# Kernel optimization log

Hardware: AMD Instinct MI355X
Metric: run time of the kernel (lower is better)

Reference implementation:

```python
import jax, jax.numpy as jnp
import numpy as np

HIDDEN = 32
INPUT = 1
B, T = 512, 2048


def setup_inputs() -> dict:
    key = jax.random.key(0)
    ks = jax.random.split(key, 12)
    s = 1.0 / np.sqrt(HIDDEN)  # torch RNN init scale
    u = lambda k, shape: jax.random.uniform(k, shape, jnp.float32, -s, s)
    return {
        "x": jax.random.normal(ks[0], (B, T, INPUT), jnp.float32),
        "hidden": jax.random.normal(ks[1], (2, B, HIDDEN), jnp.float32),
        # layer 0 (input_size=1)
        "W_ih0": u(ks[2], (HIDDEN, INPUT)),
        "W_hh0": u(ks[3], (HIDDEN, HIDDEN)),
        "b_ih0": u(ks[4], (HIDDEN,)),
        "b_hh0": u(ks[5], (HIDDEN,)),
        # layer 1 (input_size=HIDDEN)
        "W_ih1": u(ks[6], (HIDDEN, HIDDEN)),
        "W_hh1": u(ks[7], (HIDDEN, HIDDEN)),
        "b_ih1": u(ks[8], (HIDDEN,)),
        "b_hh1": u(ks[9], (HIDDEN,)),
        # output projection fc: Linear(HIDDEN, 1)
        "W_fc": u(ks[10], (1, HIDDEN)),
        "b_fc": u(ks[11], (1,)),
    }


def reference(x, hidden, W_ih0, W_hh0, b_ih0, b_hh0, W_ih1, W_hh1, b_ih1, b_hh1, W_fc, b_fc):
    # x: [B, T, 1], hidden: [2, B, H]. Vanilla tanh RNN, 2 layers, batch_first.
    xs = jnp.swapaxes(x, 0, 1)  # [T, B, 1] for scan over time

    def step(carry, x_t):
        h0, h1 = carry
        h0 = jnp.tanh(x_t @ W_ih0.T + b_ih0 + h0 @ W_hh0.T + b_hh0)
        h1 = jnp.tanh(h0 @ W_ih1.T + b_ih1 + h1 @ W_hh1.T + b_hh1)
        return (h0, h1), h1

    (h0_f, h1_f), ys = jax.lax.scan(step, (hidden[0], hidden[1]), xs)  # ys: [T, B, H]
    # fc applied per timestep in torch loop == one batched matmul here (same math)
    outs = ys @ W_fc.T + b_fc                     # [T, B, 1]
    outs = jnp.swapaxes(outs, 0, 1)               # [B, T, 1]
    hidden_out = jnp.stack([h0_f, h1_f], axis=0)  # [2, B, H] (detached in torch)
    return outs, hidden_out
```

## Files before the change

kernel.cpp:

```cpp
#include <hip/hip_runtime.h>

#define TT 2048
#define HH 32
#define BB 512
#define SCL 2.8853900817779268f

typedef float f32x2 __attribute__((ext_vector_type(2)));

#define PKFMA(acc, a, b) asm("v_pk_fma_f32 %0, %1, %2, %0" : "+v"(acc) : "v"(a), "v"(b))

__device__ __forceinline__ float tanh2(float s) {
    float e;
    asm("v_exp_f32 %0, %1" : "=v"(e) : "v"(s));
    float r = __builtin_amdgcn_rcpf(e + 1.0f);
    return fmaf(-2.0f, r, 1.0f);
}

__global__ __launch_bounds__(64) void rnn_fused(
    const float* __restrict__ x,
    const float* __restrict__ hid,
    const float* __restrict__ W_ih0,
    const float* __restrict__ W_hh0,
    const float* __restrict__ b_ih0,
    const float* __restrict__ b_hh0,
    const float* __restrict__ W_ih1,
    const float* __restrict__ W_hh1,
    const float* __restrict__ b_ih1,
    const float* __restrict__ b_hh1,
    const float* __restrict__ W_fc,
    const float* __restrict__ b_fc,
    float* __restrict__ out)
{
    const int lane   = (int)threadIdx.x;
    const int i      = lane & 31;
    const bool lower = lane < 32;
    const int b      = (int)blockIdx.x;

    __shared__ __align__(16) float sh[64];
    __shared__ float xs[32];

    const float* rowA = lower ? (W_hh0 + i * HH) : (W_ih1 + i * HH);
    const float* rowB = lower ? W_fc             : (W_hh1 + i * HH);
    const float  sclB = lower ? 1.0f : SCL;
    f32x2 wA[16], wB[16];
#pragma unroll
    for (int j = 0; j < 16; ++j) {
        wA[j] = f32x2{SCL * rowA[2 * j], SCL * rowA[2 * j + 1]};
        wB[j] = f32x2{sclB * rowB[2 * j], sclB * rowB[2 * j + 1]};
    }
    const float wx   = lower ? (SCL * W_ih0[i]) : 0.0f;
    const float bias = SCL * (lower ? (b_ih0[i] + b_hh0[i])
                                    : (b_ih1[i] + b_hh1[i]));
    const float sel  = lower ? 0.0f : 1.0f;
    const float bfc  = b_fc[0];

    const float h_init = lower ? hid[b * HH + i] : hid[BB * HH + b * HH + i];
    sh[lane] = h_init;

    const float* xrow = x + b * TT;
    float* orow = out + b * TT;

    xs[i] = xrow[i];
    float xnxt = xrow[32 + i];

    float hn = h_init;

    float4 q[16];
    auto LOADQ = [&]() {
#pragma unroll
        for (int m = 0; m < 16; ++m) q[m] = *(const float4*)&sh[4 * m];
    };
    LOADQ();

    auto STEP = [&](int kidx, bool do_store, int off) {
        float xv = xs[kidx];
        f32x2 A0 = {bias, 0.f}, A1 = {0.f, 0.f};
        f32x2 B0 = {0.f, 0.f},  B1 = {0.f, 0.f};
#pragma unroll
        for (int m = 0; m < 8; ++m) {
            f32x2 qa = {q[m].x, q[m].y}, qb = {q[m].z, q[m].w};
            PKFMA(A0, wA[2 * m], qa);
            PKFMA(A1, wA[2 * m + 1], qb);
        }
#pragma unroll
        for (int m = 0; m < 8; ++m) {
            f32x2 qa = {q[8 + m].x, q[8 + m].y}, qb = {q[8 + m].z, q[8 + m].w};
            PKFMA(B0, wB[2 * m], qa);
            PKFMA(B1, wB[2 * m + 1], qb);
        }
        f32x2 As = A0 + A1, Bs = B0 + B1;
        float s1 = As.x + As.y;
        float s2 = Bs.x + Bs.y;
        float pre = fmaf(sel, s2, fmaf(wx, xv, s1));
        float h = tanh2(pre);
        sh[lane] = h;
        hn = h;
        if (do_store && lane == 0) orow[off] = s2 + bfc;
        LOADQ();
    };

    {
        float xv = xs[0];
        f32x2 A0 = {bias, 0.f}, A1 = {0.f, 0.f};
#pragma unroll
        for (int m = 0; m < 8; ++m) {
            f32x2 qa = {q[m].x, q[m].y}, qb = {q[m].z, q[m].w};
            PKFMA(A0, wA[2 * m], qa);
            PKFMA(A1, wA[2 * m + 1], qb);
        }
        f32x2 As = A0 + A1;
        float h0new = tanh2(fmaf(wx, xv, As.x + As.y));
        float hw = lower ? h0new : h_init;
        sh[lane] = hw;
        if (lower) hn = h0new;
        LOADQ();
    }

#pragma unroll
    for (int k = 1; k < 32; ++k) {
        STEP(k, k >= 2, k - 2);
    }
    xs[i] = xnxt;
    xnxt = xrow[64 + i];

    for (int tb = 1; tb < 64; ++tb) {
        const int base = tb * 32;
#pragma unroll
        for (int k = 0; k < 32; ++k) {
            STEP(k, true, base + k - 2);
        }
        xs[i] = xnxt;
        int nidx = (tb + 2) * 32 + i;
        if (nidx >= TT) nidx = TT - 1;
        xnxt = xrow[nidx];
    }

    const float h0_fin = hn;

    STEP(0, true, TT - 2);

    {
        f32x2 B0 = {0.f, 0.f}, B1 = {0.f, 0.f};
#pragma unroll
        for (int m = 0; m < 8; ++m) {
            f32x2 qa = {q[8 + m].x, q[8 + m].y}, qb = {q[8 + m].z, q[8 + m].w};
            PKFMA(B0, wB[2 * m], qa);
            PKFMA(B1, wB[2 * m + 1], qb);
        }
        f32x2 Bs = B0 + B1;
        if (lane == 0) orow[TT - 1] = (Bs.x + Bs.y) + bfc;
    }

    if (lower) {
        out[BB * TT + b * HH + i] = h0_fin;
    } else {
        out[BB * TT + BB * HH + b * HH + i] = hn;
    }
}

extern "C" void kernel_launch(void* const* d_in, const int* in_sizes, int n_in,
                              void* d_out, int out_size, void* d_ws, size_t ws_size,
                              hipStream_t stream) {
    const float* xp    = (const float*)d_in[0];
    const float* hid   = (const float*)d_in[1];
    const float* Wih0  = (const float*)d_in[2];
    const float* Whh0  = (const float*)d_in[3];
    const float* bih0  = (const float*)d_in[4];
    const float* bhh0  = (const float*)d_in[5];
    const float* Wih1  = (const float*)d_in[6];
    const float* Whh1  = (const float*)d_in[7];
    const float* bih1  = (const float*)d_in[8];
    const float* bhh1  = (const float*)d_in[9];
    const float* Wfc   = (const float*)d_in[10];
    const float* bfc   = (const float*)d_in[11];
    float* outp        = (float*)d_out;

    rnn_fused<<<BB, 64, 0, stream>>>(xp, hid, Wih0, Whh0, bih0, bhh0,
                                     Wih1, Whh1, bih1, bhh1, Wfc, bfc, outp);
}
```

Before: 372.9 us.

## Split each RNN step into two half-phases with separate LDS exchanges

Each timestep now runs as two phases. First, all 64 lanes compute the layer-0-style dot product and tanh, write the result to LDS and reload the lower half. Then they compute the second dot product, apply a second tanh, write to LDS and reload the upper half. Layer-0 lanes republish h0 so the skewed pipeline's data dependencies become shorter chains with interleaved LDS traffic. The cost is an extra tanh and extra LDS write/read round trips per step, and the wavefront-level ordering of LDS accesses without barriers is subtle.

Measured after the change: 446.8 us. +19.8%, slower.

```diff
diff --git a/kernel.cpp b/kernel.cpp
--- a/kernel.cpp
+++ b/kernel.cpp
@@ -51,7 +51,6 @@
     const float wx   = lower ? (SCL * W_ih0[i]) : 0.0f;
     const float bias = SCL * (lower ? (b_ih0[i] + b_hh0[i])
                                     : (b_ih1[i] + b_hh1[i]));
-    const float sel  = lower ? 0.0f : 1.0f;
     const float bfc  = b_fc[0];
 
     const float h_init = lower ? hid[b * HH + i] : hid[BB * HH + b * HH + i];
@@ -65,38 +64,45 @@
 
     float hn = h_init;
 
-    float4 q[16];
-    auto LOADQ = [&]() {
+    float4 a[8], bq[8];
 #pragma unroll
-        for (int m = 0; m < 16; ++m) q[m] = *(const float4*)&sh[4 * m];
-    };
-    LOADQ();
+    for (int m = 0; m < 8; ++m) a[m]  = *(const float4*)&sh[4 * m];
+#pragma unroll
+    for (int m = 0; m < 8; ++m) bq[m] = *(const float4*)&sh[32 + 4 * m];
 
-    auto STEP = [&](int kidx, bool do_store, int off) {
-        float xv = xs[kidx];
+    auto ITER = [&](int k, bool do_store, int off) {
+        float xv = xs[k];
         f32x2 A0 = {bias, 0.f}, A1 = {0.f, 0.f};
-        f32x2 B0 = {0.f, 0.f},  B1 = {0.f, 0.f};
 #pragma unroll
         for (int m = 0; m < 8; ++m) {
-            f32x2 qa = {q[m].x, q[m].y}, qb = {q[m].z, q[m].w};
+            f32x2 qa = {a[m].x, a[m].y}, qb = {a[m].z, a[m].w};
             PKFMA(A0, wA[2 * m], qa);
             PKFMA(A1, wA[2 * m + 1], qb);
         }
+        f32x2 As = A0 + A1;
+        float s1 = As.x + As.y;
+        float h0c = tanh2(fmaf(wx, xv, s1));
+        float ew = lower ? h0c : hn;
+        sh[lane] = ew;
+#pragma unroll
+        for (int m = 0; m < 8; ++m) a[m] = *(const float4*)&sh[4 * m];
+
+        f32x2 B0 = {0.f, 0.f}, B1 = {0.f, 0.f};
 #pragma unroll
         for (int m = 0; m < 8; ++m) {
-            f32x2 qa = {q[8 + m].x, q[8 + m].y}, qb = {q[8 + m].z, q[8 + m].w};
+            f32x2 qa = {bq[m].x, bq[m].y}, qb = {bq[m].z, bq[m].w};
             PKFMA(B0, wB[2 * m], qa);
             PKFMA(B1, wB[2 * m + 1], qb);
         }
-        f32x2 As = A0 + A1, Bs = B0 + B1;
-        float s1 = As.x + As.y;
+        f32x2 Bs = B0 + B1;
         float s2 = Bs.x + Bs.y;
-        float pre = fmaf(sel, s2, fmaf(wx, xv, s1));
-        float h = tanh2(pre);
-        sh[lane] = h;
-        hn = h;
+        float h1c = tanh2(s1 + s2);
+        float lw = lower ? h0c : h1c;
+        sh[lane] = lw;
+#pragma unroll
+        for (int m = 0; m < 8; ++m) bq[m] = *(const float4*)&sh[32 + 4 * m];
+        hn = lw;
         if (do_store && lane == 0) orow[off] = s2 + bfc;
-        LOADQ();
     };
 
     {
@@ -104,21 +110,22 @@
         f32x2 A0 = {bias, 0.f}, A1 = {0.f, 0.f};
 #pragma unroll
         for (int m = 0; m < 8; ++m) {
-            f32x2 qa = {q[m].x, q[m].y}, qb = {q[m].z, q[m].w};
+            f32x2 qa = {a[m].x, a[m].y}, qb = {a[m].z, a[m].w};
             PKFMA(A0, wA[2 * m], qa);
             PKFMA(A1, wA[2 * m + 1], qb);
         }
         f32x2 As = A0 + A1;
-        float h0new = tanh2(fmaf(wx, xv, As.x + As.y));
-        float hw = lower ? h0new : h_init;
-        sh[lane] = hw;
-        if (lower) hn = h0new;
-        LOADQ();
+        float h0c = tanh2(fmaf(wx, xv, As.x + As.y));
+        float ew = lower ? h0c : hn;
+        sh[lane] = ew;
+#pragma unroll
+        for (int m = 0; m < 8; ++m) a[m] = *(const float4*)&sh[4 * m];
+        hn = ew;
     }
 
 #pragma unroll
     for (int k = 1; k < 32; ++k) {
-        STEP(k, k >= 2, k - 2);
+        ITER(k, k >= 2, k - 2);
     }
     xs[i] = xnxt;
     xnxt = xrow[64 + i];
@@ -127,7 +134,7 @@
         const int base = tb * 32;
 #pragma unroll
         for (int k = 0; k < 32; ++k) {
-            STEP(k, true, base + k - 2);
+            ITER(k, true, base + k - 2);
         }
         xs[i] = xnxt;
         int nidx = (tb + 2) * 32 + i;
@@ -137,13 +144,13 @@
 
     const float h0_fin = hn;
 
-    STEP(0, true, TT - 2);
+    ITER(0, true, TT - 2);
 
     {
         f32x2 B0 = {0.f, 0.f}, B1 = {0.f, 0.f};
 #pragma unroll
         for (int m = 0; m < 8; ++m) {
-            f32x2 qa = {q[8 + m].x, q[8 + m].y}, qb = {q[8 + m].z, q[8 + m].w};
+            f32x2 qa = {bq[m].x, bq[m].y}, qb = {bq[m].z, bq[m].w};
             PKFMA(B0, wB[2 * m], qa);
             PKFMA(B1, wB[2 * m + 1], qb);
         }
```

## Process two batch rows per wavefront with interleaved independent recurrences

Applied to the files above, without the earlier changes.

Each 64-lane block now handles two batch elements, interleaving their time-step recurrences so that one chain's FMA/tanh/LDS latency can overlap with the other's. The grid is halved to 256 blocks, so each block reuses the same weight registers across two sequences. This raises ILP within the serial dependency chain but doubles register use for the q arrays. With 256 CUs on MI355X, halving the grid leaves fewer waves than CUs, so per-wave throughput must improve enough to make up for it.

After: 703.9 us. 88.8% more time.

```diff
diff --git a/kernel.cpp b/kernel.cpp
--- a/kernel.cpp
+++ b/kernel.cpp
@@ -34,10 +34,11 @@
     const int lane   = (int)threadIdx.x;
     const int i      = lane & 31;
     const bool lower = lane < 32;
-    const int b      = (int)blockIdx.x;
-
-    __shared__ __align__(16) float sh[64];
-    __shared__ float xs[32];
+    const int bA     = (int)blockIdx.x * 2;
+    const int bB     = bA + 1;
+
+    __shared__ __align__(16) float shA[64], shB[64];
+    __shared__ float xsA[32], xsB[32];
 
     const float* rowA = lower ? (W_hh0 + i * HH) : (W_ih1 + i * HH);
     const float* rowB = lower ? W_fc             : (W_hh1 + i * HH);
@@ -54,26 +55,32 @@
     const float sel  = lower ? 0.0f : 1.0f;
     const float bfc  = b_fc[0];
 
-    const float h_init = lower ? hid[b * HH + i] : hid[BB * HH + b * HH + i];
-    sh[lane] = h_init;
-
-    const float* xrow = x + b * TT;
-    float* orow = out + b * TT;
-
-    xs[i] = xrow[i];
-    float xnxt = xrow[32 + i];
-
-    float hn = h_init;
-
-    float4 q[16];
-    auto LOADQ = [&]() {
-#pragma unroll
-        for (int m = 0; m < 16; ++m) q[m] = *(const float4*)&sh[4 * m];
-    };
-    LOADQ();
-
-    auto STEP = [&](int kidx, bool do_store, int off) {
-        float xv = xs[kidx];
+    const float h_initA = lower ? hid[bA * HH + i] : hid[BB * HH + bA * HH + i];
+    const float h_initB = lower ? hid[bB * HH + i] : hid[BB * HH + bB * HH + i];
+    shA[lane] = h_initA;
+    shB[lane] = h_initB;
+
+    const float* xrowA = x + bA * TT;
+    const float* xrowB = x + bB * TT;
+    float* orowA = out + bA * TT;
+    float* orowB = out + bB * TT;
+
+    xsA[i] = xrowA[i];
+    xsB[i] = xrowB[i];
+    float xnxtA = xrowA[32 + i];
+    float xnxtB = xrowB[32 + i];
+
+    float hnA = h_initA, hnB = h_initB;
+
+    float4 qA[16], qB[16];
+#pragma unroll
+    for (int m = 0; m < 16; ++m) qA[m] = *(const float4*)&shA[4 * m];
+#pragma unroll
+    for (int m = 0; m < 16; ++m) qB[m] = *(const float4*)&shB[4 * m];
+
+    auto STEP = [&](float4* q, float& hn, float* shp, const float* xsp,
+                    float* orowp, int k, bool do_store, int off) {
+        float xv = xsp[k];
         f32x2 A0 = {bias, 0.f}, A1 = {0.f, 0.f};
         f32x2 B0 = {0.f, 0.f},  B1 = {0.f, 0.f};
 #pragma unroll
@@ -93,14 +100,16 @@
         float s2 = Bs.x + Bs.y;
         float pre = fmaf(sel, s2, fmaf(wx, xv, s1));
         float h = tanh2(pre);
-        sh[lane] = h;
+        shp[lane] = h;
         hn = h;
-        if (do_store && lane == 0) orow[off] = s2 + bfc;
-        LOADQ();
+        if (do_store && lane == 0) orowp[off] = s2 + bfc;
+#pragma unroll
+        for (int m = 0; m < 16; ++m) q[m] = *(const float4*)&shp[4 * m];
     };
 
-    {
-        float xv = xs[0];
+    auto PEEL = [&](float4* q, float& hn, float* shp, const float* xsp,
+                    float h_init_) {
+        float xv = xsp[0];
         f32x2 A0 = {bias, 0.f}, A1 = {0.f, 0.f};
 #pragma unroll
         for (int m = 0; m < 8; ++m) {
@@ -109,37 +118,44 @@
             PKFMA(A1, wA[2 * m + 1], qb);
         }
         f32x2 As = A0 + A1;
-        float h0new = tanh2(fmaf(wx, xv, As.x + As.y));
-        float hw = lower ? h0new : h_init;
-        sh[lane] = hw;
-        if (lower) hn = h0new;
-        LOADQ();
-    }
+        float h0c = tanh2(fmaf(wx, xv, As.x + As.y));
+        float ew = lower ? h0c : h_init_;
+        shp[lane] = ew;
+        hn = ew;
+#pragma unroll
+        for (int m = 0; m < 16; ++m) q[m] = *(const float4*)&shp[4 * m];
+    };
+    PEEL(qA, hnA, shA, xsA, h_initA);
+    PEEL(qB, hnB, shB, xsB, h_initB);
 
 #pragma unroll
     for (int k = 1; k < 32; ++k) {
-        STEP(k, k >= 2, k - 2);
-    }
-    xs[i] = xnxt;
-    xnxt = xrow[64 + i];
+        STEP(qA, hnA, shA, xsA, orowA, k, k >= 2, k - 2);
+        STEP(qB, hnB, shB, xsB, orowB, k, k >= 2, k - 2);
+    }
+    xsA[i] = xnxtA;  xnxtA = xrowA[64 + i];
+    xsB[i] = xnxtB;  xnxtB = xrowB[64 + i];
 
     for (int tb = 1; tb < 64; ++tb) {
         const int base = tb * 32;
 #pragma unroll
         for (int k = 0; k < 32; ++k) {
-            STEP(k, true, base + k - 2);
-        }
-        xs[i] = xnxt;
+            STEP(qA, hnA, shA, xsA, orowA, k, true, base + k - 2);
+            STEP(qB, hnB, shB, xsB, orowB, k, true, base + k - 2);
+        }
         int nidx = (tb + 2) * 32 + i;
         if (nidx >= TT) nidx = TT - 1;
-        xnxt = xrow[nidx];
-    }
-
-    const float h0_fin = hn;
-
-    STEP(0, true, TT - 2);
-
-    {
+        xsA[i] = xnxtA;  xnxtA = xrowA[nidx];
+        xsB[i] = xnxtB;  xnxtB = xrowB[nidx];
+    }
+
+    const float h0_finA = hnA;
+    const float h0_finB = hnB;
+
+    STEP(qA, hnA, shA, xsA, orowA, 0, true, TT - 2);
+    STEP(qB, hnB, shB, xsB, orowB, 0, true, TT - 2);
+
+    auto FINFC = [&](const float4* q, float* orowp) {
         f32x2 B0 = {0.f, 0.f}, B1 = {0.f, 0.f};
 #pragma unroll
         for (int m = 0; m < 8; ++m) {
@@ -148,13 +164,17 @@
             PKFMA(B1, wB[2 * m + 1], qb);
         }
         f32x2 Bs = B0 + B1;
-        if (lane == 0) orow[TT - 1] = (Bs.x + Bs.y) + bfc;
-    }
+        if (lane == 0) orowp[TT - 1] = (Bs.x + Bs.y) + bfc;
+    };
+    FINFC(qA, orowA);
+    FINFC(qB, orowB);
 
     if (lower) {
-        out[BB * TT + b * HH + i] = h0_fin;
+        out[BB * TT + bA * HH + i] = h0_finA;
+        out[BB * TT + bB * HH + i] = h0_finB;
     } else {
-        out[BB * TT + BB * HH + b * HH + i] = hn;
+        out[BB * TT + BB * HH + bA * HH + i] = hnA;
+        out[BB * TT + BB * HH + bB * HH + i] = hnB;
     }
 }
 
@@ -175,6 +195,6 @@
     const float* bfc   = (const float*)d_in[11];
     float* outp        = (float*)d_out;
 
-    rnn_fused<<<BB, 64, 0, stream>>>(xp, hid, Wih0, Whh0, bih0, bhh0,
-                                     Wih1, Whh1, bih1, bhh1, Wfc, bfc, outp);
+    rnn_fused<<<BB / 2, 64, 0, stream>>>(xp, hid, Wih0, Whh0, bih0, bhh0,
+                                         Wih1, Whh1, bih1, bhh1, Wfc, bfc, outp);
 }
```

## Skew layers by two steps, split W_ih1 across halves, batch FC output

Applied to the files above, without the earlier changes.

Restructures the per-step work so each half-wave does fewer FMAs on the critical path. Layer 1 now reads layer-0 hidden states from a small 4-deep history buffer, with layer 0 running two steps ahead, and the W_ih1 product is split across both halves and combined with a cross-half shuffle. The per-step FC dot product and lane-0 store are replaced by writing h1 to a 32-step LDS ring, which is reduced and stored in bulk every 32 steps. This trades extra LDS traffic and a shuffle per step for a shorter per-step dependency chain.

Result: slower. 426.7 us (+14.4%).

```diff
diff --git a/kernel.cpp b/kernel.cpp
--- a/kernel.cpp
+++ b/kernel.cpp
@@ -16,7 +16,7 @@
     return fmaf(-2.0f, r, 1.0f);
 }
 
-__global__ __launch_bounds__(64) void rnn_fused(
+__global__ __launch_bounds__(64, 1) void rnn_fused(
     const float* __restrict__ x,
     const float* __restrict__ hid,
     const float* __restrict__ W_ih0,
@@ -38,21 +38,28 @@
 
     __shared__ __align__(16) float sh[64];
     __shared__ float xs[32];
-
-    const float* rowA = lower ? (W_hh0 + i * HH) : (W_ih1 + i * HH);
-    const float* rowB = lower ? W_fc             : (W_hh1 + i * HH);
-    const float  sclB = lower ? 1.0f : SCL;
-    f32x2 wA[16], wB[16];
-#pragma unroll
-    for (int j = 0; j < 16; ++j) {
+    __shared__ __align__(16) float ring[32][68];
+    __shared__ __align__(16) float h0hist[4][32];
+
+    const float* rowA = lower ? (W_hh0 + i * HH) : (W_hh1 + i * HH);
+    const float* rowS = W_ih1 + i * HH + (lower ? 0 : 16);
+    const float* wfp  = W_fc + (lower ? 0 : 16);
+    f32x2 wA[16], wS[8], wf[8];
+#pragma unroll
+    for (int j = 0; j < 16; ++j)
         wA[j] = f32x2{SCL * rowA[2 * j], SCL * rowA[2 * j + 1]};
-        wB[j] = f32x2{sclB * rowB[2 * j], sclB * rowB[2 * j + 1]};
+#pragma unroll
+    for (int j = 0; j < 8; ++j) {
+        wS[j] = f32x2{SCL * rowS[2 * j], SCL * rowS[2 * j + 1]};
+        wf[j] = f32x2{wfp[2 * j], wfp[2 * j + 1]};
     }
     const float wx   = lower ? (SCL * W_ih0[i]) : 0.0f;
     const float bias = SCL * (lower ? (b_ih0[i] + b_hh0[i])
                                     : (b_ih1[i] + b_hh1[i]));
-    const float sel  = lower ? 0.0f : 1.0f;
     const float bfc  = b_fc[0];
+    const int   qb   = lower ? 0 : 32;
+    const int   rb2  = lower ? 0 : 16;
+    const int   fb   = 32 + (lower ? 0 : 16);
 
     const float h_init = lower ? hid[b * HH + i] : hid[BB * HH + b * HH + i];
     sh[lane] = h_init;
@@ -60,99 +67,112 @@
     const float* xrow = x + b * TT;
     float* orow = out + b * TT;
 
-    xs[i] = xrow[i];
-    float xnxt = xrow[32 + i];
+    xs[i] = xrow[2 + i];
+    float xnxt = xrow[34 + i];
 
     float hn = h_init;
 
-    float4 q[16];
-    auto LOADQ = [&]() {
-#pragma unroll
-        for (int m = 0; m < 16; ++m) q[m] = *(const float4*)&sh[4 * m];
-    };
-    LOADQ();
-
-    auto STEP = [&](int kidx, bool do_store, int off) {
-        float xv = xs[kidx];
+    float4 q[8];
+#pragma unroll
+    for (int m = 0; m < 8; ++m) q[m] = *(const float4*)&sh[qb + 4 * m];
+
+    {
+        float xv0 = xrow[0];
         f32x2 A0 = {bias, 0.f}, A1 = {0.f, 0.f};
-        f32x2 B0 = {0.f, 0.f},  B1 = {0.f, 0.f};
 #pragma unroll
         for (int m = 0; m < 8; ++m) {
-            f32x2 qa = {q[m].x, q[m].y}, qb = {q[m].z, q[m].w};
+            f32x2 qa = {q[m].x, q[m].y}, qc = {q[m].z, q[m].w};
             PKFMA(A0, wA[2 * m], qa);
-            PKFMA(A1, wA[2 * m + 1], qb);
-        }
+            PKFMA(A1, wA[2 * m + 1], qc);
+        }
+        f32x2 As = A0 + A1;
+        float h = tanh2(fmaf(wx, xv0, As.x + As.y));
+        sh[lane] = lower ? h : h_init;
+        if (lower) h0hist[0][i] = h;
+#pragma unroll
+        for (int m = 0; m < 8; ++m) q[m] = *(const float4*)&sh[qb + 4 * m];
+    }
+    {
+        float xv1 = xrow[1];
+        f32x2 A0 = {bias, 0.f}, A1 = {0.f, 0.f};
 #pragma unroll
         for (int m = 0; m < 8; ++m) {
-            f32x2 qa = {q[8 + m].x, q[8 + m].y}, qb = {q[8 + m].z, q[8 + m].w};
-            PKFMA(B0, wB[2 * m], qa);
-            PKFMA(B1, wB[2 * m + 1], qb);
-        }
-        f32x2 As = A0 + A1, Bs = B0 + B1;
+            f32x2 qa = {q[m].x, q[m].y}, qc = {q[m].z, q[m].w};
+            PKFMA(A0, wA[2 * m], qa);
+            PKFMA(A1, wA[2 * m + 1], qc);
+        }
+        f32x2 As = A0 + A1;
+        float h = tanh2(fmaf(wx, xv1, As.x + As.y));
+        sh[lane] = lower ? h : h_init;
+        if (lower) h0hist[1][i] = h;
+#pragma unroll
+        for (int m = 0; m < 8; ++m) q[m] = *(const float4*)&sh[qb + 4 * m];
+    }
+
+    auto STEP = [&](int k) {
+        float4 rq[4];
+#pragma unroll
+        for (int m = 0; m < 4; ++m)
+            rq[m] = *(const float4*)&h0hist[k & 3][rb2 + 4 * m];
+        f32x2 A0 = {bias, 0.f}, A1 = {0.f, 0.f};
+#pragma unroll
+        for (int m = 0; m < 8; ++m) {
+            f32x2 qa = {q[m].x, q[m].y}, qc = {q[m].z, q[m].w};
+            PKFMA(A0, wA[2 * m], qa);
+            PKFMA(A1, wA[2 * m + 1], qc);
+        }
+        f32x2 S0 = {0.f, 0.f}, S1 = {0.f, 0.f};
+#pragma unroll
+        for (int m = 0; m < 4; ++m) {
+            f32x2 ra = {rq[m].x, rq[m].y}, rc = {rq[m].z, rq[m].w};
+            PKFMA(S0, wS[2 * m], ra);
+            PKFMA(S1, wS[2 * m + 1], rc);
+        }
+        f32x2 Ss = S0 + S1;
+        float s2p = Ss.x + Ss.y;
+        float s2 = s2p + __shfl_xor(s2p, 32);
+        f32x2 As = A0 + A1;
         float s1 = As.x + As.y;
-        float s2 = Bs.x + Bs.y;
-        float pre = fmaf(sel, s2, fmaf(wx, xv, s1));
+        float xv = xs[k];
+        float pre = lower ? fmaf(wx, xv, s1) : (s1 + s2);
         float h = tanh2(pre);
         sh[lane] = h;
+        float* wp = lower ? &h0hist[(k + 2) & 3][i] : &ring[k][lane];
+        *wp = h;
         hn = h;
-        if (do_store && lane == 0) orow[off] = s2 + bfc;
-        LOADQ();
+#pragma unroll
+        for (int m = 0; m < 8; ++m) q[m] = *(const float4*)&sh[qb + 4 * m];
     };
 
-    {
-        float xv = xs[0];
-        f32x2 A0 = {bias, 0.f}, A1 = {0.f, 0.f};
-#pragma unroll
-        for (int m = 0; m < 8; ++m) {
-            f32x2 qa = {q[m].x, q[m].y}, qb = {q[m].z, q[m].w};
-            PKFMA(A0, wA[2 * m], qa);
-            PKFMA(A1, wA[2 * m + 1], qb);
-        }
-        f32x2 As = A0 + A1;
-        float h0new = tanh2(fmaf(wx, xv, As.x + As.y));
-        float hw = lower ? h0new : h_init;
-        sh[lane] = hw;
-        if (lower) hn = h0new;
-        LOADQ();
-    }
-
-#pragma unroll
-    for (int k = 1; k < 32; ++k) {
-        STEP(k, k >= 2, k - 2);
-    }
-    xs[i] = xnxt;
-    xnxt = xrow[64 + i];
-
-    for (int tb = 1; tb < 64; ++tb) {
-        const int base = tb * 32;
-#pragma unroll
-        for (int k = 0; k < 32; ++k) {
-            STEP(k, true, base + k - 2);
-        }
+    auto FLUSH = [&](int base) {
+        f32x2 F0 = {0.f, 0.f}, F1 = {0.f, 0.f};
+#pragma unroll
+        for (int m = 0; m < 4; ++m) {
+            float4 r = *(const float4*)&ring[i][fb + 4 * m];
+            f32x2 ra = {r.x, r.y}, rc = {r.z, r.w};
+            PKFMA(F0, wf[2 * m], ra);
+            PKFMA(F1, wf[2 * m + 1], rc);
+        }
+        f32x2 Fs = F0 + F1;
+        float fp = Fs.x + Fs.y;
+        float ff = fp + __shfl_xor(fp, 32) + bfc;
+        if (lower) orow[base + i] = ff;
+    };
+
+    for (int G = 0; G < 64; ++G) {
+        if (G) FLUSH(32 * (G - 1));
+#pragma unroll
+        for (int k = 0; k < 32; ++k) STEP(k);
         xs[i] = xnxt;
-        int nidx = (tb + 2) * 32 + i;
+        int nidx = 32 * (G + 2) + 2 + i;
         if (nidx >= TT) nidx = TT - 1;
         xnxt = xrow[nidx];
     }
-
-    const float h0_fin = hn;
-
-    STEP(0, true, TT - 2);
-
-    {
-        f32x2 B0 = {0.f, 0.f}, B1 = {0.f, 0.f};
-#pragma unroll
-        for (int m = 0; m < 8; ++m) {
-            f32x2 qa = {q[8 + m].x, q[8 + m].y}, qb = {q[8 + m].z, q[8 + m].w};
-            PKFMA(B0, wB[2 * m], qa);
-            PKFMA(B1, wB[2 * m + 1], qb);
-        }
-        f32x2 Bs = B0 + B1;
-        if (lane == 0) orow[TT - 1] = (Bs.x + Bs.y) + bfc;
-    }
-
+    FLUSH(32 * 63);
+
+    float h0f = h0hist[3][i];
     if (lower) {
-        out[BB * TT + b * HH + i] = h0_fin;
+        out[BB * TT + b * HH + i] = h0f;
     } else {
         out[BB * TT + BB * HH + b * HH + i] = hn;
     }
```
